# Kernel optimization log

Hardware: AMD Instinct MI355X
Metric: run time of the kernel (lower is better)

The kernel has to match this reference:

```python
import jax, jax.numpy as jnp
import numpy as np

D = 192      # d_model
DE = 96      # d_edge
H = 8        # n_heads
DH = D // H  # d_head = 24
DF = 2 * D   # ff hidden = 384
N = 25000
E = 400000


def _layernorm(x, s, b, eps=1e-5):
    m = jnp.mean(x, axis=-1, keepdims=True)
    v = jnp.var(x, axis=-1, keepdims=True)
    return (x - m) * jax.lax.rsqrt(v + eps) * s + b


def setup_inputs() -> dict:
    key = jax.random.key(0)
    ks = jax.random.split(key, 12)
    sc = lambda d: 1.0 / np.sqrt(d)
    inp = {
        "x": jax.random.normal(ks[0], (N, D), jnp.float32),
        "edge_feat": jax.random.normal(ks[1], (E, DE), jnp.float32),
        "edge_index": jax.random.randint(ks[2], (2, E), 0, N, jnp.int64),
        # attention projections (stored [d_in, d_out], applied as x @ W)
        "Wq": jax.random.normal(ks[3], (D, D), jnp.float32) * sc(D),
        "Wk": jax.random.normal(ks[4], (D, D), jnp.float32) * sc(D),
        "Wv": jax.random.normal(ks[5], (D, D), jnp.float32) * sc(D),
        "We": jax.random.normal(ks[6], (DE, H), jnp.float32) * sc(DE),
        "Wo": jax.random.normal(ks[7], (D, D), jnp.float32) * sc(D),
        "bo": jnp.zeros((D,), jnp.float32),
        "Wg": jax.random.normal(ks[8], (2 * D, D), jnp.float32) * sc(2 * D),
        "bg": jnp.zeros((D,), jnp.float32),
        "ln1_s": jnp.ones((D,), jnp.float32),
        "ln1_b": jnp.zeros((D,), jnp.float32),
        "Wf1": jax.random.normal(ks[9], (D, DF), jnp.float32) * sc(D),
        "bf1": jnp.zeros((DF,), jnp.float32),
        "Wf2": jax.random.normal(ks[10], (DF, D), jnp.float32) * sc(DF),
        "bf2": jnp.zeros((D,), jnp.float32),
        "ln2_s": jnp.ones((D,), jnp.float32),
        "ln2_b": jnp.zeros((D,), jnp.float32),
    }
    return inp


def reference(x, edge_feat, edge_index, Wq, Wk, Wv, We, Wo, bo, Wg, bg,
              ln1_s, ln1_b, Wf1, bf1, Wf2, bf2, ln2_s, ln2_b):
    src, dst = edge_index[0], edge_index[1]
    n = x.shape[0]
    # per-edge gathered projections: [E, H, DH]
    q = (x[dst] @ Wq).reshape(-1, H, DH)
    k = (x[src] @ Wk).reshape(-1, H, DH)
    v = (x[src] @ Wv).reshape(-1, H, DH)
    score = jnp.sum(q * k, axis=-1) / np.sqrt(DH) + edge_feat @ We  # [E, H]
    # segment softmax over incoming edges of each dst node
    mx = jax.ops.segment_max(score, dst, num_segments=n)           # [N, H]
    alpha = jnp.exp(score - mx[dst])                                # [E, H]
    den = jax.ops.segment_sum(alpha, dst, num_segments=n)          # [N, H]
    num = jax.ops.segment_sum(alpha[..., None] * v, dst, num_segments=n)  # [N, H, DH]
    agg = (num / (den[:, :, None] + 1e-8)).reshape(n, D)
    o = agg @ Wo + bo
    g = jax.nn.sigmoid(jnp.concatenate([o, x], axis=-1) @ Wg + bg)
    y = _layernorm(g * o + (1.0 - g) * x, ln1_s, ln1_b)
    ff = jax.nn.silu(y @ Wf1 + bf1) @ Wf2 + bf2
    return _layernorm(y + ff, ln2_s, ln2_b)
```

## Files before the change

### kernel.cpp

```cpp
#include <hip/hip_runtime.h>
#include <cstdint>
#include <cstddef>

#define LOG2E 1.4426950408889634f

constexpr int Dm  = 192;
constexpr int DEe = 96;

typedef unsigned short u16;
typedef __attribute__((ext_vector_type(8))) short short8v;
typedef __attribute__((ext_vector_type(4))) float f32x4;

__device__ __forceinline__ u16 f2bf(float f) {
    uint32_t u = __builtin_bit_cast(uint32_t, f);
    uint32_t r = (u + 0x7FFF + ((u >> 16) & 1)) >> 16;
    return (u16)r;
}
__device__ __forceinline__ float bf2f(u16 h) {
    uint32_t u = ((uint32_t)h) << 16;
    return __builtin_bit_cast(float, u);
}

__global__ void zero_ints(int* __restrict__ p, int n) {
    int i = blockIdx.x * blockDim.x + threadIdx.x;
    if (i < n) p[i] = 0;
}

__global__ void count_deg(const int* __restrict__ ei, int E, int* __restrict__ deg) {
    int e = blockIdx.x * blockDim.x + threadIdx.x;
    if (e < E) atomicAdd(&deg[ei[E + e]], 1);
}

__global__ __launch_bounds__(1024) void scan_kernel(const int* __restrict__ deg, int N,
                                                    int* __restrict__ offs) {
    __shared__ int sp[1024];
    int t = threadIdx.x;
    int per = (N + 1023) >> 10;
    int base = t * per;
    int sum = 0;
    for (int i = 0; i < per; ++i) {
        int idx = base + i;
        if (idx < N) sum += deg[idx];
    }
    sp[t] = sum;
    __syncthreads();
    for (int off = 1; off < 1024; off <<= 1) {
        int v = (t >= off) ? sp[t - off] : 0;
        __syncthreads();
        sp[t] += v;
        __syncthreads();
    }
    int run = sp[t] - sum;
    for (int i = 0; i < per; ++i) {
        int idx = base + i;
        if (idx < N) { offs[idx] = run; run += deg[idx]; }
    }
    if (t == 1023) offs[N] = sp[1023];
}

__global__ void xconv(const float* __restrict__ x, int n4, u16* __restrict__ xb) {
    int i = blockIdx.x * blockDim.x + threadIdx.x;
    if (i >= n4) return;
    float4 v = ((const float4*)x)[i];
    ushort4 o;
    o.x = f2bf(v.x); o.y = f2bf(v.y); o.z = f2bf(v.z); o.w = f2bf(v.w);
    ((ushort4*)xb)[i] = o;
}

__global__ void prep_w(const float* __restrict__ Wq, const float* __restrict__ Wk,
                       const float* __restrict__ Wv, const float* __restrict__ Wo,
                       const float* __restrict__ Wg, const float* __restrict__ Wf1,
                       const float* __restrict__ Wf2,
                       u16* __restrict__ Wqkvt, u16* __restrict__ Wot,
                       u16* __restrict__ Wgt, u16* __restrict__ Wf1t,
                       u16* __restrict__ Wf2t) {
    int idx = blockIdx.x * blockDim.x + threadIdx.x;
    if (idx < 110592) {
        int n = idx / 192, k = idx % 192;
        const float* W = n < 192 ? Wq : (n < 384 ? Wk : Wv);
        Wqkvt[idx] = f2bf(W[(size_t)k * 192 + (n % 192)]);
    } else if (idx < 147456) {
        int i = idx - 110592;
        int n = i / 192, k = i % 192;
        Wot[i] = f2bf(Wo[(size_t)k * 192 + n]);
    } else if (idx < 221184) {
        int i = idx - 147456;
        int n = i / 384, k = i % 384;
        Wgt[i] = f2bf(Wg[(size_t)k * 192 + n]);
    } else if (idx < 294912) {
        int i = idx - 221184;
        int n = i / 192, k = i % 192;
        Wf1t[i] = f2bf(Wf1[(size_t)k * 384 + n]);
    } else if (idx < 368640) {
        int i = idx - 294912;
        int n = i / 384, k = i % 384;
        Wf2t[i] = f2bf(Wf2[(size_t)k * 192 + n]);
    }
}

__global__ __launch_bounds__(256) void edge_prep(
    const int* __restrict__ ei, int E,
    const float* __restrict__ ef, const float* __restrict__ We,
    const int* __restrict__ offs, int* __restrict__ cur,
    float* __restrict__ scb, int* __restrict__ sbuf)
{
    __shared__ float We_s[DEe * 8];
    __shared__ float ef_s[32][100];
    int tid = threadIdx.x;
    for (int i = tid; i < DEe * 8; i += 256) We_s[i] = We[i];
    int e0 = blockIdx.x * 32;
    #pragma unroll
    for (int rep = 0; rep < 3; ++rep) {
        int idx = tid + 256 * rep;
        int el = idx / 24, c4 = idx % 24;
        int e = e0 + el;
        float4 v = make_float4(0.f, 0.f, 0.f, 0.f);
        if (e < E) v = *(const float4*)&ef[(size_t)e * DEe + c4 * 4];
        *(float4*)&ef_s[el][c4 * 4] = v;
    }
    __syncthreads();
    int el = tid >> 3, h = tid & 7;
    int e = e0 + el;
    if (e >= E) return;
    float epj = 0.f;
    #pragma unroll 8
    for (int i = 0; i < DEe; ++i) epj += ef_s[el][i] * We_s[i * 8 + h];

    int lane = tid & 63;
    int pos = 0;
    if (h == 0) {
        int dst = ei[E + e];
        pos = offs[dst] + atomicAdd(&cur[dst], 1);
    }
    pos = __shfl(pos, lane & 56, 64);
    scb[(size_t)pos * 8 + h] = epj * LOG2E;
    if (h == 0) sbuf[pos] = ei[e];
}

__global__ __launch_bounds__(256) void agg_fused(
    const u16* __restrict__ qkv, const float* __restrict__ scb,
    const int* __restrict__ sbuf, const int* __restrict__ offs,
    int N, u16* __restrict__ aggb)
{
    int node = blockIdx.x * 4 + (threadIdx.x >> 6);
    if (node >= N) return;
    int lane = threadIdx.x & 63;
    int h = lane >> 3;
    int di = (3 * lane) >> 1;
    int odd = lane & 1;

    const uint32_t* qrow = (const uint32_t*)(qkv + (size_t)node * 576);
    uint32_t qd0 = qrow[di], qd1 = qrow[di + 1];
    float q0, q1, q2;
    if (!odd) { q0 = bf2f(qd0 & 0xffff); q1 = bf2f(qd0 >> 16); q2 = bf2f(qd1 & 0xffff); }
    else      { q0 = bf2f(qd0 >> 16);    q1 = bf2f(qd1 & 0xffff); q2 = bf2f(qd1 >> 16); }

    float den = 0.f, a0 = 0.f, a1 = 0.f, a2 = 0.f;
    int beg = offs[node], end = offs[node + 1];

    uint32_t kd0_n = 0, kd1_n = 0, vd0_n = 0, vd1_n = 0; float ep_n = 0.f;
    if (beg < end) {
        int src = sbuf[beg];
        const uint32_t* kr = (const uint32_t*)(qkv + (size_t)src * 576 + 192);
        kd0_n = kr[di]; kd1_n = kr[di + 1];
        const uint32_t* vr = (const uint32_t*)(qkv + (size_t)src * 576 + 384);
        vd0_n = vr[di]; vd1_n = vr[di + 1];
        ep_n = scb[(size_t)beg * 8 + h];
    }

    for (int idx = beg; idx < end; ++idx) {
        uint32_t kd0 = kd0_n, kd1 = kd1_n, vd0 = vd0_n, vd1 = vd1_n;
        float ep = ep_n;
        if (idx + 1 < end) {
            int src = sbuf[idx + 1];
            const uint32_t* kr = (const uint32_t*)(qkv + (size_t)src * 576 + 192);
            kd0_n = kr[di]; kd1_n = kr[di + 1];
            const uint32_t* vr = (const uint32_t*)(qkv + (size_t)src * 576 + 384);
            vd0_n = vr[di]; vd1_n = vr[di + 1];
            ep_n = scb[(size_t)(idx + 1) * 8 + h];
        }
        float k0, k1, k2, v0, v1, v2;
        if (!odd) {
            k0 = bf2f(kd0 & 0xffff); k1 = bf2f(kd0 >> 16); k2 = bf2f(kd1 & 0xffff);
            v0 = bf2f(vd0 & 0xffff); v1 = bf2f(vd0 >> 16); v2 = bf2f(vd1 & 0xffff);
        } else {
            k0 = bf2f(kd0 >> 16); k1 = bf2f(kd1 & 0xffff); k2 = bf2f(kd1 >> 16);
            v0 = bf2f(vd0 >> 16); v1 = bf2f(vd1 & 0xffff); v2 = bf2f(vd1 >> 16);
        }
        float pd = q0 * k0 + q1 * k1 + q2 * k2;
        pd += __shfl_xor(pd, 1, 64);
        pd += __shfl_xor(pd, 2, 64);
        pd += __shfl_xor(pd, 4, 64);
        float p = exp2f(pd * 0.2944885836f + ep);
        den += p;
        a0 += p * v0; a1 += p * v1; a2 += p * v2;
    }
    float rden = 1.f / (den + 1e-8f);
    u16* og = aggb + (size_t)node * Dm;
    int b0 = 3 * lane;
    og[b0]     = f2bf(a0 * rden);
    og[b0 + 1] = f2bf(a1 * rden);
    og[b0 + 2] = f2bf(a2 * rden);
}

__global__ __launch_bounds__(512) void qkv_gemm(
    const u16* __restrict__ xb, int M,
    const u16* __restrict__ Wt, u16* __restrict__ qkvb)
{
    int tid = threadIdx.x;
    int m0 = blockIdx.x * 128, n0 = blockIdx.y * 192;
    int w = tid >> 6, lane = tid & 63;
    int wr = w >> 2, wc = w & 3;
    int c16 = lane & 15, hi2 = lane >> 4, kof = hi2 * 8;
    int rbase = m0 + wr * 64;

    int rcm[4];
    #pragma unroll
    for (int mr = 0; mr < 4; ++mr) {
        int r = rbase + mr * 16 + c16;
        rcm[mr] = r < M ? r : M - 1;
    }

    f32x4 acc[4][3];
    #pragma unroll
    for (int mr = 0; mr < 4; ++mr)
        #pragma unroll
        for (int nr = 0; nr < 3; ++nr) acc[mr][nr] = (f32x4)(0.f);

    #pragma unroll 1
    for (int ks = 0; ks < 6; ++ks) {
        short8v af[4], bfr[3];
        #pragma unroll
        for (int mr = 0; mr < 4; ++mr)
            af[mr] = *(const short8v*)(xb + (size_t)rcm[mr] * 192 + ks * 32 + kof);
        #pragma unroll
        for (int nr = 0; nr < 3; ++nr)
            bfr[nr] = *(const short8v*)(Wt + (size_t)(n0 + wc * 48 + nr * 16 + c16) * 192 + ks * 32 + kof);
        #pragma unroll
        for (int mr = 0; mr < 4; ++mr)
            #pragma unroll
            for (int nr = 0; nr < 3; ++nr)
                acc[mr][nr] = __builtin_amdgcn_mfma_f32_16x16x32_bf16(
                    af[mr], bfr[nr], acc[mr][nr], 0, 0, 0);
    }

    #pragma unroll
    for (int mr = 0; mr < 4; ++mr)
        #pragma unroll
        for (int reg = 0; reg < 4; ++reg) {
            int r = rbase + mr * 16 + hi2 * 4 + reg;
            if (r >= M) continue;
            #pragma unroll
            for (int nr = 0; nr < 3; ++nr)
                qkvb[(size_t)r * 576 + n0 + wc * 48 + nr * 16 + c16] =
                    f2bf(acc[mr][nr][reg]);
        }
}

__global__ __launch_bounds__(512) void chain_fused(
    const u16* __restrict__ aggb, const u16* __restrict__ xb, int M,
    const u16* __restrict__ Wot, const float* __restrict__ bo,
    const u16* __restrict__ Wgt, const float* __restrict__ bg,
    const float* __restrict__ l1s, const float* __restrict__ l1b,
    const u16* __restrict__ Wf1t, const float* __restrict__ bf1,
    const u16* __restrict__ Wf2t, const float* __restrict__ bf2,
    const float* __restrict__ l2s, const float* __restrict__ l2b,
    float* __restrict__ out)
{
    __shared__ __align__(16) short Ybuf[128 * 200];
    __shared__ __align__(16) short Fbuf[128 * 392];
    __shared__ float red[2][4][128];

    int tid = threadIdx.x;
    int m0 = blockIdx.x * 128;
    int w = tid >> 6, lane = tid & 63;
    int wr = w >> 2, wc = w & 3;
    int c16 = lane & 15, hi2 = lane >> 4, kof = hi2 * 8;
    int rbase = m0 + wr * 64;
    int lbase = wr * 64;

    int rcm[4];
    #pragma unroll
    for (int mr = 0; mr < 4; ++mr) {
        int r = rbase + mr * 16 + c16;
        rcm[mr] = r < M ? r : M - 1;
    }

    f32x4 oacc[4][3];
    #pragma unroll
    for (int mr = 0; mr < 4; ++mr)
        #pragma unroll
        for (int nr = 0; nr < 3; ++nr) oacc[mr][nr] = (f32x4)(0.f);
    #pragma unroll 1
    for (int ks = 0; ks < 6; ++ks) {
        short8v af[4], bfr[3];
        #pragma unroll
        for (int mr = 0; mr < 4; ++mr)
            af[mr] = *(const short8v*)(aggb + (size_t)rcm[mr] * 192 + ks * 32 + kof);
        #pragma unroll
        for (int nr = 0; nr < 3; ++nr)
            bfr[nr] = *(const short8v*)(Wot + (size_t)(wc * 48 + nr * 16 + c16) * 192 + ks * 32 + kof);
        #pragma unroll
        for (int mr = 0; mr < 4; ++mr)
            #pragma unroll
            for (int nr = 0; nr < 3; ++nr)
                oacc[mr][nr] = __builtin_amdgcn_mfma_f32_16x16x32_bf16(
                    af[mr], bfr[nr], oacc[mr][nr], 0, 0, 0);
    }
    #pragma unroll
    for (int nr = 0; nr < 3; ++nr) {
        int col = wc * 48 + nr * 16 + c16;
        float b = bo[col];
        #pragma unroll
        for (int mr = 0; mr < 4; ++mr)
            #pragma unroll
            for (int reg = 0; reg < 4; ++reg) {
                oacc[mr][nr][reg] += b;
                int row = lbase + mr * 16 + hi2 * 4 + reg;
                Ybuf[row * 200 + col] = (short)f2bf(oacc[mr][nr][reg]);
            }
    }
    __syncthreads();

    f32x4 zacc[4][3];
    #pragma unroll
    for (int mr = 0; mr < 4; ++mr)
        #pragma unroll
        for (int nr = 0; nr < 3; ++nr) zacc[mr][nr] = (f32x4)(0.f);
    #pragma unroll 1
    for (int ks = 0; ks < 6; ++ks) {
        short8v af[4], bfr[3];
        #pragma unroll
        for (int mr = 0; mr < 4; ++mr)
            af[mr] = *(const short8v*)&Ybuf[(lbase + mr * 16 + c16) * 200 + ks * 32 + kof];
        #pragma unroll
        for (int nr = 0; nr < 3; ++nr)
            bfr[nr] = *(const short8v*)(Wgt + (size_t)(wc * 48 + nr * 16 + c16) * 384 + ks * 32 + kof);
        #pragma unroll
        for (int mr = 0; mr < 4; ++mr)
            #pragma unroll
            for (int nr = 0; nr < 3; ++nr)
                zacc[mr][nr] = __builtin_amdgcn_mfma_f32_16x16x32_bf16(
                    af[mr], bfr[nr], zacc[mr][nr], 0, 0, 0);
    }
    #pragma unroll 1
    for (int ks = 0; ks < 6; ++ks) {
        short8v af[4], bfr[3];
        #pragma unroll
        for (int mr = 0; mr < 4; ++mr)
            af[mr] = *(const short8v*)(xb + (size_t)rcm[mr] * 192 + ks * 32 + kof);
        #pragma unroll
        for (int nr = 0; nr < 3; ++nr)
            bfr[nr] = *(const short8v*)(Wgt + (size_t)(wc * 48 + nr * 16 + c16) * 384 + 192 + ks * 32 + kof);
        #pragma unroll
        for (int mr = 0; mr < 4; ++mr)
            #pragma unroll
            for (int nr = 0; nr < 3; ++nr)
                zacc[mr][nr] = __builtin_amdgcn_mfma_f32_16x16x32_bf16(
                    af[mr], bfr[nr], zacc[mr][nr], 0, 0, 0);
    }
    float s1p[4][4], s2p[4][4];
    #pragma unroll
    for (int mr = 0; mr < 4; ++mr)
        #pragma unroll
        for (int reg = 0; reg < 4; ++reg) {
            int gr = rbase + mr * 16 + hi2 * 4 + reg;
            int rcR = gr < M ? gr : M - 1;
            float s1 = 0.f, s2 = 0.f;
            #pragma unroll
            for (int nr = 0; nr < 3; ++nr) {
                int col = wc * 48 + nr * 16 + c16;
                float z = zacc[mr][nr][reg] + bg[col];
                float g = 1.f / (1.f + expf(-z));
                float xv = bf2f(xb[(size_t)rcR * 192 + col]);
                float val = g * oacc[mr][nr][reg] + (1.f - g) * xv;
                zacc[mr][nr][reg] = val;
                s1 += val; s2 += val * val;
            }
            #pragma unroll
            for (int mS = 1; mS < 16; mS <<= 1) {
                s1 += __shfl_xor(s1, mS, 64);
                s2 += __shfl_xor(s2, mS, 64);
            }
            s1p[mr][reg] = s1; s2p[mr][reg] = s2;
        }
    if (c16 == 0) {
        #pragma unroll
        for (int mr = 0; mr < 4; ++mr)
            #pragma unroll
            for (int reg = 0; reg < 4; ++reg) {
                int rowIdx = lbase + mr * 16 + hi2 * 4 + reg;
                red[0][wc][rowIdx] = s1p[mr][reg];
                red[1][wc][rowIdx] = s2p[mr][reg];
            }
    }
    __syncthreads();
    #pragma unroll
    for (int mr = 0; mr < 4; ++mr)
        #pragma unroll
        for (int reg = 0; reg < 4; ++reg) {
            int rowIdx = lbase + mr * 16 + hi2 * 4 + reg;
            float S1 = red[0][0][rowIdx] + red[0][1][rowIdx] + red[0][2][rowIdx] + red[0][3][rowIdx];
            float S2 = red[1][0][rowIdx] + red[1][1][rowIdx] + red[1][2][rowIdx] + red[1][3][rowIdx];
            float mean = S1 * (1.f / 192.f);
            float var  = S2 * (1.f / 192.f) - mean * mean;
            float inv  = rsqrtf(var + 1e-5f);
            #pragma unroll
            for (int nr = 0; nr < 3; ++nr) {
                int col = wc * 48 + nr * 16 + c16;
                float yv = (zacc[mr][nr][reg] - mean) * inv * l1s[col] + l1b[col];
                Ybuf[rowIdx * 200 + col] = (short)f2bf(yv);
            }
        }
    __syncthreads();

    f32x4 tacc[4][6];
    #pragma unroll
    for (int mr = 0; mr < 4; ++mr)
        #pragma unroll
        for (int nr = 0; nr < 6; ++nr) tacc[mr][nr] = (f32x4)(0.f);
    #pragma unroll 1
    for (int ks = 0; ks < 6; ++ks) {
        short8v af[4], bfr[6];
        #pragma unroll
        for (int mr = 0; mr < 4; ++mr)
            af[mr] = *(const short8v*)&Ybuf[(lbase + mr * 16 + c16) * 200 + ks * 32 + kof];
        #pragma unroll
        for (int nr = 0; nr < 6; ++nr)
            bfr[nr] = *(const short8v*)(Wf1t + (size_t)(wc * 96 + nr * 16 + c16) * 192 + ks * 32 + kof);
        #pragma unroll
        for (int mr = 0; mr < 4; ++mr)
            #pragma unroll
            for (int nr = 0; nr < 6; ++nr)
                tacc[mr][nr] = __builtin_amdgcn_mfma_f32_16x16x32_bf16(
                    af[mr], bfr[nr], tacc[mr][nr], 0, 0, 0);
    }
    #pragma unroll
    for (int nr = 0; nr < 6; ++nr) {
        int col = wc * 96 + nr * 16 + c16;
        float b = bf1[col];
        #pragma unroll
        for (int mr = 0; mr < 4; ++mr)
            #pragma unroll
            for (int reg = 0; reg < 4; ++reg) {
                float z = tacc[mr][nr][reg] + b;
                float t = z / (1.f + expf(-z));
                int row = lbase + mr * 16 + hi2 * 4 + reg;
                Fbuf[row * 392 + col] = (short)f2bf(t);
            }
    }
    __syncthreads();

    f32x4 facc[4][3];
    #pragma unroll
    for (int mr = 0; mr < 4; ++mr)
        #pragma unroll
        for (int nr = 0; nr < 3; ++nr) facc[mr][nr] = (f32x4)(0.f);
    #pragma unroll 1
    for (int ks = 0; ks < 12; ++ks) {
        short8v af[4], bfr[3];
        #pragma unroll
        for (int mr = 0; mr < 4; ++mr)
            af[mr] = *(const short8v*)&Fbuf[(lbase + mr * 16 + c16) * 392 + ks * 32 + kof];
        #pragma unroll
        for (int nr = 0; nr < 3; ++nr)
            bfr[nr] = *(const short8v*)(Wf2t + (size_t)(wc * 48 + nr * 16 + c16) * 384 + ks * 32 + kof);
        #pragma unroll
        for (int mr = 0; mr < 4; ++mr)
            #pragma unroll
            for (int nr = 0; nr < 3; ++nr)
                facc[mr][nr] = __builtin_amdgcn_mfma_f32_16x16x32_bf16(
                    af[mr], bfr[nr], facc[mr][nr], 0, 0, 0);
    }
    float s1q[4][4], s2q[4][4];
    #pragma unroll
    for (int mr = 0; mr < 4; ++mr)
        #pragma unroll
        for (int reg = 0; reg < 4; ++reg) {
            int rowIdx = lbase + mr * 16 + hi2 * 4 + reg;
            float s1 = 0.f, s2 = 0.f;
            #pragma unroll
            for (int nr = 0; nr < 3; ++nr) {
                int col = wc * 48 + nr * 16 + c16;
                float val = facc[mr][nr][reg] + bf2[col] + bf2f((u16)Ybuf[rowIdx * 200 + col]);
                facc[mr][nr][reg] = val;
                s1 += val; s2 += val * val;
            }
            #pragma unroll
            for (int mS = 1; mS < 16; mS <<= 1) {
                s1 += __shfl_xor(s1, mS, 64);
                s2 += __shfl_xor(s2, mS, 64);
            }
            s1q[mr][reg] = s1; s2q[mr][reg] = s2;
        }
    if (c16 == 0) {
        #pragma unroll
        for (int mr = 0; mr < 4; ++mr)
            #pragma unroll
            for (int reg = 0; reg < 4; ++reg) {
                int rowIdx = lbase + mr * 16 + hi2 * 4 + reg;
                red[0][wc][rowIdx] = s1q[mr][reg];
                red[1][wc][rowIdx] = s2q[mr][reg];
            }
    }
    __syncthreads();
    #pragma unroll
    for (int mr = 0; mr < 4; ++mr)
        #pragma unroll
        for (int reg = 0; reg < 4; ++reg) {
            int rowIdx = lbase + mr * 16 + hi2 * 4 + reg;
            int r = m0 + rowIdx;
            if (r >= M) continue;
            float S1 = red[0][0][rowIdx] + red[0][1][rowIdx] + red[0][2][rowIdx] + red[0][3][rowIdx];
            float S2 = red[1][0][rowIdx] + red[1][1][rowIdx] + red[1][2][rowIdx] + red[1][3][rowIdx];
            float mean = S1 * (1.f / 192.f);
            float var  = S2 * (1.f / 192.f) - mean * mean;
            float inv  = rsqrtf(var + 1e-5f);
            #pragma unroll
            for (int nr = 0; nr < 3; ++nr) {
                int col = wc * 48 + nr * 16 + c16;
                out[(size_t)r * 192 + col] =
                    (facc[mr][nr][reg] - mean) * inv * l2s[col] + l2b[col];
            }
        }
}

extern "C" void kernel_launch(void* const* d_in, const int* in_sizes, int n_in,
                              void* d_out, int out_size, void* d_ws, size_t ws_size,
                              hipStream_t stream) {
    const float* x   = (const float*)d_in[0];
    const float* ef  = (const float*)d_in[1];
    const int*   ei  = (const int*)d_in[2];
    const float* Wq  = (const float*)d_in[3];
    const float* Wk  = (const float*)d_in[4];
    const float* Wv  = (const float*)d_in[5];
    const float* We  = (const float*)d_in[6];
    const float* Wo  = (const float*)d_in[7];
    const float* bo  = (const float*)d_in[8];
    const float* Wg  = (const float*)d_in[9];
    const float* bg  = (const float*)d_in[10];
    const float* l1s = (const float*)d_in[11];
    const float* l1b = (const float*)d_in[12];
    const float* Wf1 = (const float*)d_in[13];
    const float* bf1 = (const float*)d_in[14];
    const float* Wf2 = (const float*)d_in[15];
    const float* bf2 = (const float*)d_in[16];
    const float* l2s = (const float*)d_in[17];
    const float* l2b = (const float*)d_in[18];

    int N = in_sizes[0] / Dm;
    int E = in_sizes[1] / DEe;
    float* out = (float*)d_out;

    char* wp = (char*)d_ws;
    auto alloc = [&](size_t bytes) -> void* {
        void* p = wp;
        wp += (bytes + 255) & ~(size_t)255;
        return p;
    };
    size_t NF = (size_t)N * Dm;
    u16*   xb     = (u16*)alloc(NF * 2);
    u16*   qkvb   = (u16*)alloc((size_t)N * 576 * 2);
    u16*   aggb   = (u16*)alloc(NF * 2);
    float* scb    = (float*)alloc((size_t)E * 8 * 4);
    int*   sbuf   = (int*)  alloc((size_t)E * 4);
    int*   degcur = (int*)  alloc((size_t)2 * N * 4);
    int*   offs   = (int*)  alloc((size_t)(N + 1) * 4);
    u16*   Wqkvt  = (u16*)alloc((size_t)576 * 192 * 2);
    u16*   Wot    = (u16*)alloc((size_t)192 * 192 * 2);
    u16*   Wgt    = (u16*)alloc((size_t)192 * 384 * 2);
    u16*   Wf1t   = (u16*)alloc((size_t)384 * 192 * 2);
    u16*   Wf2t   = (u16*)alloc((size_t)192 * 384 * 2);
    int* deg = degcur;
    int* cur = degcur + N;

    int gm128 = (N + 127) / 128;

    prep_w<<<dim3(1440), 256, 0, stream>>>(Wq, Wk, Wv, Wo, Wg, Wf1, Wf2,
        Wqkvt, Wot, Wgt, Wf1t, Wf2t);
    xconv<<<dim3((N * Dm / 4 + 255) / 256), 256, 0, stream>>>(x, N * Dm / 4, xb);
    zero_ints<<<dim3((2 * N + 255) / 256), 256, 0, stream>>>(degcur, 2 * N);
    count_deg<<<dim3((E + 255) / 256), 256, 0, stream>>>(ei, E, deg);
    scan_kernel<<<dim3(1), 1024, 0, stream>>>(deg, N, offs);

    qkv_gemm<<<dim3(gm128, 3), 512, 0, stream>>>(xb, N, Wqkvt, qkvb);

    edge_prep<<<dim3((E + 31) / 32), 256, 0, stream>>>(ei, E, ef, We,
        offs, cur, scb, sbuf);
    agg_fused<<<dim3((N + 3) / 4), 256, 0, stream>>>(qkvb, scb, sbuf, offs, N, aggb);

    chain_fused<<<dim3(gm128), 512, 0, stream>>>(aggb, xb, N,
        Wot, bo, Wgt, bg, l1s, l1b, Wf1t, bf1, Wf2t, bf2, l2s, l2b, out);
}
```

Baseline: 285.9 us.

## Split fused post-attention chain into three kernels and use packed bf16 conversion

The single chain_fused kernel, which held a large LDS footprint (Ybuf plus Fbuf) and ran on only ~196 blocks, is split into chainA (out-proj, gate, LN1), ff1_gemm (FF1 + SiLU) and ff2_gemm (FF2 + residual + LN2). Intermediates y and the FF hidden activations now round-trip through global memory as bf16. The split frees LDS per block, which could raise occupancy. Float-to-bf16 conversions also switch to the hardware v_cvt_pk_bf16_f32 instruction. The trade-off is extra global traffic and two more kernel launches.

```diff
diff --git a/kernel.cpp b/kernel.cpp
--- a/kernel.cpp
+++ b/kernel.cpp
@@ -19,6 +19,11 @@
 __device__ __forceinline__ float bf2f(u16 h) {
     uint32_t u = ((uint32_t)h) << 16;
     return __builtin_bit_cast(float, u);
+}
+__device__ __forceinline__ uint32_t cvtpk_bf16(float lo, float hi) {
+    uint32_t r;
+    asm("v_cvt_pk_bf16_f32 %0, %1, %2" : "=v"(r) : "v"(lo), "v"(hi));
+    return r;
 }
 
 __global__ void zero_ints(int* __restrict__ p, int n) {
@@ -62,8 +67,11 @@
     int i = blockIdx.x * blockDim.x + threadIdx.x;
     if (i >= n4) return;
     float4 v = ((const float4*)x)[i];
+    uint32_t p0 = cvtpk_bf16(v.x, v.y);
+    uint32_t p1 = cvtpk_bf16(v.z, v.w);
     ushort4 o;
-    o.x = f2bf(v.x); o.y = f2bf(v.y); o.z = f2bf(v.z); o.w = f2bf(v.w);
+    o.x = (u16)(p0 & 0xffff); o.y = (u16)(p0 >> 16);
+    o.z = (u16)(p1 & 0xffff); o.w = (u16)(p1 >> 16);
     ((ushort4*)xb)[i] = o;
 }
 
@@ -247,28 +255,26 @@
     #pragma unroll
     for (int mr = 0; mr < 4; ++mr)
         #pragma unroll
-        for (int reg = 0; reg < 4; ++reg) {
-            int r = rbase + mr * 16 + hi2 * 4 + reg;
-            if (r >= M) continue;
-            #pragma unroll
-            for (int nr = 0; nr < 3; ++nr)
-                qkvb[(size_t)r * 576 + n0 + wc * 48 + nr * 16 + c16] =
-                    f2bf(acc[mr][nr][reg]);
-        }
-}
-
-__global__ __launch_bounds__(512) void chain_fused(
+        for (int nr = 0; nr < 3; ++nr) {
+            uint32_t p0 = cvtpk_bf16(acc[mr][nr][0], acc[mr][nr][1]);
+            uint32_t p1 = cvtpk_bf16(acc[mr][nr][2], acc[mr][nr][3]);
+            int r0 = rbase + mr * 16 + hi2 * 4;
+            int col = n0 + wc * 48 + nr * 16 + c16;
+            if (r0     < M) qkvb[(size_t)(r0    ) * 576 + col] = (u16)(p0 & 0xffff);
+            if (r0 + 1 < M) qkvb[(size_t)(r0 + 1) * 576 + col] = (u16)(p0 >> 16);
+            if (r0 + 2 < M) qkvb[(size_t)(r0 + 2) * 576 + col] = (u16)(p1 & 0xffff);
+            if (r0 + 3 < M) qkvb[(size_t)(r0 + 3) * 576 + col] = (u16)(p1 >> 16);
+        }
+}
+
+__global__ __launch_bounds__(512) void chainA(
     const u16* __restrict__ aggb, const u16* __restrict__ xb, int M,
     const u16* __restrict__ Wot, const float* __restrict__ bo,
     const u16* __restrict__ Wgt, const float* __restrict__ bg,
     const float* __restrict__ l1s, const float* __restrict__ l1b,
-    const u16* __restrict__ Wf1t, const float* __restrict__ bf1,
-    const u16* __restrict__ Wf2t, const float* __restrict__ bf2,
-    const float* __restrict__ l2s, const float* __restrict__ l2b,
-    float* __restrict__ out)
+    u16* __restrict__ yb)
 {
     __shared__ __align__(16) short Ybuf[128 * 200];
-    __shared__ __align__(16) short Fbuf[128 * 392];
     __shared__ float red[2][4][128];
 
     int tid = threadIdx.x;
@@ -312,13 +318,17 @@
         int col = wc * 48 + nr * 16 + c16;
         float b = bo[col];
         #pragma unroll
-        for (int mr = 0; mr < 4; ++mr)
-            #pragma unroll
-            for (int reg = 0; reg < 4; ++reg) {
-                oacc[mr][nr][reg] += b;
-                int row = lbase + mr * 16 + hi2 * 4 + reg;
-                Ybuf[row * 200 + col] = (short)f2bf(oacc[mr][nr][reg]);
-            }
+        for (int mr = 0; mr < 4; ++mr) {
+            #pragma unroll
+            for (int reg = 0; reg < 4; ++reg) oacc[mr][nr][reg] += b;
+            uint32_t p0 = cvtpk_bf16(oacc[mr][nr][0], oacc[mr][nr][1]);
+            uint32_t p1 = cvtpk_bf16(oacc[mr][nr][2], oacc[mr][nr][3]);
+            int row0 = lbase + mr * 16 + hi2 * 4;
+            Ybuf[(row0    ) * 200 + col] = (short)(p0 & 0xffff);
+            Ybuf[(row0 + 1) * 200 + col] = (short)(p0 >> 16);
+            Ybuf[(row0 + 2) * 200 + col] = (short)(p1 & 0xffff);
+            Ybuf[(row0 + 3) * 200 + col] = (short)(p1 >> 16);
+        }
     }
     __syncthreads();
 
@@ -400,6 +410,8 @@
         #pragma unroll
         for (int reg = 0; reg < 4; ++reg) {
             int rowIdx = lbase + mr * 16 + hi2 * 4 + reg;
+            int r = m0 + rowIdx;
+            if (r >= M) continue;
             float S1 = red[0][0][rowIdx] + red[0][1][rowIdx] + red[0][2][rowIdx] + red[0][3][rowIdx];
             float S2 = red[1][0][rowIdx] + red[1][1][rowIdx] + red[1][2][rowIdx] + red[1][3][rowIdx];
             float mean = S1 * (1.f / 192.f);
@@ -409,22 +421,42 @@
             for (int nr = 0; nr < 3; ++nr) {
                 int col = wc * 48 + nr * 16 + c16;
                 float yv = (zacc[mr][nr][reg] - mean) * inv * l1s[col] + l1b[col];
-                Ybuf[rowIdx * 200 + col] = (short)f2bf(yv);
-            }
-        }
-    __syncthreads();
+                yb[(size_t)r * 192 + col] = f2bf(yv);
+            }
+        }
+}
+
+__global__ __launch_bounds__(512) void ff1_gemm(
+    const u16* __restrict__ yb, int M,
+    const u16* __restrict__ Wf1t, const float* __restrict__ bf1,
+    u16* __restrict__ tb)
+{
+    int tid = threadIdx.x;
+    int m0 = blockIdx.x * 128;
+    int w = tid >> 6, lane = tid & 63;
+    int wr = w >> 2, wc = w & 3;
+    int c16 = lane & 15, hi2 = lane >> 4, kof = hi2 * 8;
+    int rbase = m0 + wr * 64;
+
+    int rcm[4];
+    #pragma unroll
+    for (int mr = 0; mr < 4; ++mr) {
+        int r = rbase + mr * 16 + c16;
+        rcm[mr] = r < M ? r : M - 1;
+    }
 
     f32x4 tacc[4][6];
     #pragma unroll
     for (int mr = 0; mr < 4; ++mr)
         #pragma unroll
         for (int nr = 0; nr < 6; ++nr) tacc[mr][nr] = (f32x4)(0.f);
+
     #pragma unroll 1
     for (int ks = 0; ks < 6; ++ks) {
         short8v af[4], bfr[6];
         #pragma unroll
         for (int mr = 0; mr < 4; ++mr)
-            af[mr] = *(const short8v*)&Ybuf[(lbase + mr * 16 + c16) * 200 + ks * 32 + kof];
+            af[mr] = *(const short8v*)(yb + (size_t)rcm[mr] * 192 + ks * 32 + kof);
         #pragma unroll
         for (int nr = 0; nr < 6; ++nr)
             bfr[nr] = *(const short8v*)(Wf1t + (size_t)(wc * 96 + nr * 16 + c16) * 192 + ks * 32 + kof);
@@ -435,33 +467,65 @@
                 tacc[mr][nr] = __builtin_amdgcn_mfma_f32_16x16x32_bf16(
                     af[mr], bfr[nr], tacc[mr][nr], 0, 0, 0);
     }
+
     #pragma unroll
     for (int nr = 0; nr < 6; ++nr) {
         int col = wc * 96 + nr * 16 + c16;
         float b = bf1[col];
         #pragma unroll
-        for (int mr = 0; mr < 4; ++mr)
+        for (int mr = 0; mr < 4; ++mr) {
+            float t0[4];
             #pragma unroll
             for (int reg = 0; reg < 4; ++reg) {
                 float z = tacc[mr][nr][reg] + b;
-                float t = z / (1.f + expf(-z));
-                int row = lbase + mr * 16 + hi2 * 4 + reg;
-                Fbuf[row * 392 + col] = (short)f2bf(t);
-            }
-    }
-    __syncthreads();
+                t0[reg] = z / (1.f + expf(-z));
+            }
+            uint32_t p0 = cvtpk_bf16(t0[0], t0[1]);
+            uint32_t p1 = cvtpk_bf16(t0[2], t0[3]);
+            int r0 = rbase + mr * 16 + hi2 * 4;
+            if (r0     < M) tb[(size_t)(r0    ) * 384 + col] = (u16)(p0 & 0xffff);
+            if (r0 + 1 < M) tb[(size_t)(r0 + 1) * 384 + col] = (u16)(p0 >> 16);
+            if (r0 + 2 < M) tb[(size_t)(r0 + 2) * 384 + col] = (u16)(p1 & 0xffff);
+            if (r0 + 3 < M) tb[(size_t)(r0 + 3) * 384 + col] = (u16)(p1 >> 16);
+        }
+    }
+}
+
+__global__ __launch_bounds__(512) void ff2_gemm(
+    const u16* __restrict__ tb, const u16* __restrict__ yb, int M,
+    const u16* __restrict__ Wf2t, const float* __restrict__ bf2,
+    const float* __restrict__ l2s, const float* __restrict__ l2b,
+    float* __restrict__ out)
+{
+    __shared__ float red[2][4][128];
+
+    int tid = threadIdx.x;
+    int m0 = blockIdx.x * 128;
+    int w = tid >> 6, lane = tid & 63;
+    int wr = w >> 2, wc = w & 3;
+    int c16 = lane & 15, hi2 = lane >> 4, kof = hi2 * 8;
+    int rbase = m0 + wr * 64;
+    int lbase = wr * 64;
+
+    int rcm[4];
+    #pragma unroll
+    for (int mr = 0; mr < 4; ++mr) {
+        int r = rbase + mr * 16 + c16;
+        rcm[mr] = r < M ? r : M - 1;
+    }
 
     f32x4 facc[4][3];
     #pragma unroll
     for (int mr = 0; mr < 4; ++mr)
         #pragma unroll
         for (int nr = 0; nr < 3; ++nr) facc[mr][nr] = (f32x4)(0.f);
+
     #pragma unroll 1
     for (int ks = 0; ks < 12; ++ks) {
         short8v af[4], bfr[3];
         #pragma unroll
         for (int mr = 0; mr < 4; ++mr)
-            af[mr] = *(const short8v*)&Fbuf[(lbase + mr * 16 + c16) * 392 + ks * 32 + kof];
+            af[mr] = *(const short8v*)(tb + (size_t)rcm[mr] * 384 + ks * 32 + kof);
         #pragma unroll
         for (int nr = 0; nr < 3; ++nr)
             bfr[nr] = *(const short8v*)(Wf2t + (size_t)(wc * 48 + nr * 16 + c16) * 384 + ks * 32 + kof);
@@ -472,17 +536,19 @@
                 facc[mr][nr] = __builtin_amdgcn_mfma_f32_16x16x32_bf16(
                     af[mr], bfr[nr], facc[mr][nr], 0, 0, 0);
     }
+
     float s1q[4][4], s2q[4][4];
     #pragma unroll
     for (int mr = 0; mr < 4; ++mr)
         #pragma unroll
         for (int reg = 0; reg < 4; ++reg) {
-            int rowIdx = lbase + mr * 16 + hi2 * 4 + reg;
+            int gr = rbase + mr * 16 + hi2 * 4 + reg;
+            int rr = gr < M ? gr : M - 1;
             float s1 = 0.f, s2 = 0.f;
             #pragma unroll
             for (int nr = 0; nr < 3; ++nr) {
                 int col = wc * 48 + nr * 16 + c16;
-                float val = facc[mr][nr][reg] + bf2[col] + bf2f((u16)Ybuf[rowIdx * 200 + col]);
+                float val = facc[mr][nr][reg] + bf2[col] + bf2f(yb[(size_t)rr * 192 + col]);
                 facc[mr][nr][reg] = val;
                 s1 += val; s2 += val * val;
             }
@@ -562,6 +628,8 @@
     u16*   xb     = (u16*)alloc(NF * 2);
     u16*   qkvb   = (u16*)alloc((size_t)N * 576 * 2);
     u16*   aggb   = (u16*)alloc(NF * 2);
+    u16*   yb     = (u16*)alloc(NF * 2);
+    u16*   tb     = (u16*)alloc((size_t)N * 384 * 2);
     float* scb    = (float*)alloc((size_t)E * 8 * 4);
     int*   sbuf   = (int*)  alloc((size_t)E * 4);
     int*   degcur = (int*)  alloc((size_t)2 * N * 4);
@@ -589,6 +657,8 @@
         offs, cur, scb, sbuf);
     agg_fused<<<dim3((N + 3) / 4), 256, 0, stream>>>(qkvb, scb, sbuf, offs, N, aggb);
 
-    chain_fused<<<dim3(gm128), 512, 0, stream>>>(aggb, xb, N,
-        Wot, bo, Wgt, bg, l1s, l1b, Wf1t, bf1, Wf2t, bf2, l2s, l2b, out);
-}
+    chainA<<<dim3(gm128), 512, 0, stream>>>(aggb, xb, N,
+        Wot, bo, Wgt, bg, l1s, l1b, yb);
+    ff1_gemm<<<dim3(gm128), 512, 0, stream>>>(yb, N, Wf1t, bf1, tb);
+    ff2_gemm<<<dim3(gm128), 512, 0, stream>>>(tb, yb, N, Wf2t, bf2, l2s, l2b, out);
+}
```

New measurement: 318.3 us. 11.3% more time.
